# Optimization experiments

Measured on AMD Instinct MI355X. Metric: run time of the kernel, lower is better.

The kernel has to match this reference:

```python
import jax, jax.numpy as jnp
import numpy as np

N = 80          # grid points per side
L = 2.0         # domain size, grid spans [-L//2, L//2] = [-1, 1]
NG = 4          # num_gaussians; alpha has 4*NG entries (last NG unused, as in source)


def setup_inputs() -> dict:
    key = jax.random.key(0)
    k_alpha, = jax.random.split(key, 1)
    # amplitudes/centers in [0,1): keeps 1 + sum(a_i * gaussian) strictly positive
    alpha = jax.random.uniform(k_alpha, (4 * NG,), dtype=jnp.float32)

    # 5-point Laplacian stencil matrix, identical to the double loop in _assemble_lhs:
    # A = kron(I, T) + kron(T, I), T = tridiag(-1, 2, -1)
    T = 2.0 * np.eye(N) - np.eye(N, k=1) - np.eye(N, k=-1)
    A = np.kron(np.eye(N), T) + np.kron(T, np.eye(N))

    # rhs f = func(x, y) on the meshgrid, func = sin(pi x) sin(pi y)
    xs = np.linspace(-(L // 2), L // 2, N)
    X, Y = np.meshgrid(xs, xs, indexing='ij')
    f = np.sin(np.pi * X) * np.sin(np.pi * Y)

    return {
        'alpha': alpha,
        'A': jnp.asarray(A, dtype=jnp.float32),
        'f': jnp.asarray(f.reshape(-1), dtype=jnp.float32),
    }


def reference(alpha, A, f):
    # diffusion map: 1 + sum_i a_i * exp(-((x - cx_i)^2 + (y - cy_i)^2))
    xs = jnp.linspace(-(L // 2), L // 2, N, dtype=jnp.float32)
    X, Y = jnp.meshgrid(xs, xs, indexing='ij')          # (N, N)
    amps = alpha[:NG]
    cx = alpha[NG:2 * NG]
    cy = alpha[2 * NG:3 * NG]
    # (N, N, NG) gaussian basis, contracted against amplitudes
    g = jnp.exp(-((X[..., None] - cx) ** 2 + (Y[..., None] - cy) ** 2))
    dm = 1.0 + g @ amps                                  # (N, N)
    # torch broadcasting: dm (M,) * A (M, M) scales COLUMNS of A
    M = A * dm.reshape(-1)[None, :]
    return jnp.linalg.solve(M, f)
```

## Files before the change

### kernel.cpp

```cpp
#include <hip/hip_runtime.h>
#include <math.h>


#define NN   80
#define NP   81
#define RPW  4
#define NWG  (NN / RPW)
#define NTH  (RPW * NN)
#define PIF  3.14159265358979323846f

__device__ __forceinline__ void build_sin_table(float* tbl, int tid) {
    if (tid < 2 * NP) tbl[tid] = sinf(PIF * (float)tid / (float)NP);
}

__device__ __forceinline__ void build_S(float (*Sm)[NN], const float* tbl, int tid) {
    for (int p = tid; p < NN * NN; p += NTH) {
        const int k = p / NN, i = p - k * NN;
        Sm[k][i] = tbl[((k + 1) * (i + 1)) % (2 * NP)];
    }
}

__global__ __launch_bounds__(NTH) void poisson_phase1(
    const float* __restrict__ f, float* __restrict__ u2g)
{
    __shared__ __align__(16) float Sm[NN][NN];
    __shared__ __align__(16) float Fl[NN][NN];
    __shared__ float U1[RPW][NN];
    __shared__ float tbl[2 * NP];
    __shared__ float lam[NN];

    const int tid = threadIdx.x;
    const int wg  = blockIdx.x;

    build_sin_table(tbl, tid);
    if (tid < NN) {
        const float s = sinf(PIF * (float)(tid + 1) / (2.0f * (float)NP));
        lam[tid] = 4.0f * s * s;
    }
    for (int p = tid; p < NN * NN / 4; p += NTH)
        reinterpret_cast<float4*>(&Fl[0][0])[p] =
            reinterpret_cast<const float4*>(f)[p];
    __syncthreads();
    build_S(Sm, tbl, tid);
    __syncthreads();

    const int r = tid / NN;
    const int i = tid - r * NN;
    const int a = wg * RPW + r;

    float acc = 0.0f;
    #pragma unroll 8
    for (int k = 0; k < NN; ++k) acc += Sm[a][k] * Fl[k][i];
    U1[r][i] = acc;
    __syncthreads();

    float acc2 = 0.0f;
    #pragma unroll 8
    for (int k = 0; k < NN; ++k) acc2 += U1[r][k] * Sm[k][i];
    u2g[a * NN + i] = acc2 / (lam[a] + lam[i]);
}

__global__ __launch_bounds__(NTH) void poisson_phase2(
    const float* __restrict__ alpha, const float* __restrict__ u2g,
    float* __restrict__ out)
{
    __shared__ __align__(16) float Sm[NN][NN];
    __shared__ __align__(16) float U2[NN][NN];
    __shared__ float Tl[RPW][NN];
    __shared__ float tbl[2 * NP];
    __shared__ float gyl[4][NN];
    __shared__ float gxv[RPW][4];

    const int tid = threadIdx.x;
    const int wg  = blockIdx.x;

    build_sin_table(tbl, tid);
    for (int p = tid; p < NN * NN / 4; p += NTH)
        reinterpret_cast<float4*>(&U2[0][0])[p] =
            reinterpret_cast<const float4*>(u2g)[p];
    {
        const int k = tid / NN, j = tid - k * NN;
        const float yj = -1.0f + 2.0f * (float)j / 79.0f;
        const float d  = yj - alpha[8 + k];
        gyl[k][j] = __expf(-(d * d));
    }
    if (tid < RPW * 4) {
        const int r = tid / 4, k = tid - r * 4;
        const float xi = -1.0f + 2.0f * (float)(wg * RPW + r) / 79.0f;
        const float d  = xi - alpha[4 + k];
        gxv[r][k] = alpha[k] * __expf(-(d * d));
    }
    __syncthreads();
    build_S(Sm, tbl, tid);
    __syncthreads();

    const int r   = tid / NN;
    const int j   = tid - r * NN;
    const int row = wg * RPW + r;

    float t = 0.0f;
    #pragma unroll 8
    for (int a = 0; a < NN; ++a) t += Sm[row][a] * U2[a][j];
    Tl[r][j] = t;
    __syncthreads();

    float y = 0.0f;
    #pragma unroll 8
    for (int b = 0; b < NN; ++b) y += Tl[r][b] * Sm[b][j];

    float dm = 1.0f;
    #pragma unroll
    for (int k = 0; k < 4; ++k) dm += gxv[r][k] * gyl[k][j];

    const float scale = 4.0f / ((float)NP * (float)NP);
    out[row * NN + j] = y * scale / dm;
}

extern "C" void kernel_launch(void* const* d_in, const int* in_sizes, int n_in,
                              void* d_out, int out_size, void* d_ws, size_t ws_size,
                              hipStream_t stream) {
    const float* alpha = (const float*)d_in[0];
    const float* f = (const float*)d_in[2];
    float* out = (float*)d_out;
    float* u2  = (float*)d_ws;

    hipLaunchKernelGGL(poisson_phase1, dim3(NWG), dim3(NTH), 0, stream, f, u2);
    hipLaunchKernelGGL(poisson_phase2, dim3(NWG), dim3(NTH), 0, stream, alpha, u2, out);
}
```

Before: 16.06 us.

## Register-tile the DST matmuls with float4 2x4 micro-tiles and vectorize sine-matrix build

Each of the two small matrix products per workgroup now runs on 40 threads, each computing a 2x4 register tile with float4 LDS loads, instead of 320 threads each computing one scalar dot product. The sine-matrix build uses one thread per quarter-row, with an incremental modulo index replacing a per-element division and modulo. The global-to-LDS copy is issued before the table setup to overlap latency. This cuts LDS load traffic and index arithmetic, but leaves most threads idle during the matmuls, which reduces parallelism and latency hiding.

```diff
diff --git a/kernel.cpp b/kernel.cpp
--- a/kernel.cpp
+++ b/kernel.cpp
@@ -6,17 +6,50 @@
 #define NP   81
 #define RPW  4
 #define NWG  (NN / RPW)
-#define NTH  (RPW * NN)
+#define NTH  320
 #define PIF  3.14159265358979323846f
+
+__device__ __forceinline__ void gemm2x4(const float* __restrict__ row0,
+                                        const float* __restrict__ row1,
+                                        const float (*__restrict__ Cm)[NN],
+                                        int c4, float acc[2][4])
+{
+    #pragma unroll
+    for (int r = 0; r < 2; ++r)
+        #pragma unroll
+        for (int c = 0; c < 4; ++c) acc[r][c] = 0.0f;
+
+    #pragma unroll 4
+    for (int k4 = 0; k4 < NN; k4 += 4) {
+        const float4 a0 = *reinterpret_cast<const float4*>(row0 + k4);
+        const float4 a1 = *reinterpret_cast<const float4*>(row1 + k4);
+        const float4 b0 = *reinterpret_cast<const float4*>(&Cm[k4 + 0][c4]);
+        const float4 b1 = *reinterpret_cast<const float4*>(&Cm[k4 + 1][c4]);
+        const float4 b2 = *reinterpret_cast<const float4*>(&Cm[k4 + 2][c4]);
+        const float4 b3 = *reinterpret_cast<const float4*>(&Cm[k4 + 3][c4]);
+        acc[0][0] += a0.x*b0.x; acc[0][1] += a0.x*b0.y; acc[0][2] += a0.x*b0.z; acc[0][3] += a0.x*b0.w;
+        acc[0][0] += a0.y*b1.x; acc[0][1] += a0.y*b1.y; acc[0][2] += a0.y*b1.z; acc[0][3] += a0.y*b1.w;
+        acc[0][0] += a0.z*b2.x; acc[0][1] += a0.z*b2.y; acc[0][2] += a0.z*b2.z; acc[0][3] += a0.z*b2.w;
+        acc[0][0] += a0.w*b3.x; acc[0][1] += a0.w*b3.y; acc[0][2] += a0.w*b3.z; acc[0][3] += a0.w*b3.w;
+        acc[1][0] += a1.x*b0.x; acc[1][1] += a1.x*b0.y; acc[1][2] += a1.x*b0.z; acc[1][3] += a1.x*b0.w;
+        acc[1][0] += a1.y*b1.x; acc[1][1] += a1.y*b1.y; acc[1][2] += a1.y*b1.z; acc[1][3] += a1.y*b1.w;
+        acc[1][0] += a1.z*b2.x; acc[1][1] += a1.z*b2.y; acc[1][2] += a1.z*b2.z; acc[1][3] += a1.z*b2.w;
+        acc[1][0] += a1.w*b3.x; acc[1][1] += a1.w*b3.y; acc[1][2] += a1.w*b3.z; acc[1][3] += a1.w*b3.w;
+    }
+}
 
 __device__ __forceinline__ void build_sin_table(float* tbl, int tid) {
     if (tid < 2 * NP) tbl[tid] = sinf(PIF * (float)tid / (float)NP);
 }
 
 __device__ __forceinline__ void build_S(float (*Sm)[NN], const float* tbl, int tid) {
-    for (int p = tid; p < NN * NN; p += NTH) {
-        const int k = p / NN, i = p - k * NN;
-        Sm[k][i] = tbl[((k + 1) * (i + 1)) % (2 * NP)];
+    const int k = tid >> 2, q = tid & 3;
+    const int k1 = k + 1, base = q * 20;
+    int m = (k1 * (base + 1)) % (2 * NP);
+    #pragma unroll
+    for (int ii = 0; ii < 20; ++ii) {
+        Sm[k][base + ii] = tbl[m];
+        m += k1; if (m >= 2 * NP) m -= 2 * NP;
     }
 }
 
@@ -24,40 +57,53 @@
     const float* __restrict__ f, float* __restrict__ u2g)
 {
     __shared__ __align__(16) float Sm[NN][NN];
-    __shared__ __align__(16) float Fl[NN][NN];
-    __shared__ float U1[RPW][NN];
+    __shared__ __align__(16) float Wb[NN][NN];
+    __shared__ __align__(16) float Rw[RPW][NN];
     __shared__ float tbl[2 * NP];
     __shared__ float lam[NN];
 
     const int tid = threadIdx.x;
     const int wg  = blockIdx.x;
 
+    for (int p = tid; p < NN * NN / 4; p += NTH)
+        reinterpret_cast<float4*>(&Wb[0][0])[p] =
+            reinterpret_cast<const float4*>(f)[p];
     build_sin_table(tbl, tid);
     if (tid < NN) {
         const float s = sinf(PIF * (float)(tid + 1) / (2.0f * (float)NP));
         lam[tid] = 4.0f * s * s;
     }
-    for (int p = tid; p < NN * NN / 4; p += NTH)
-        reinterpret_cast<float4*>(&Fl[0][0])[p] =
-            reinterpret_cast<const float4*>(f)[p];
     __syncthreads();
     build_S(Sm, tbl, tid);
     __syncthreads();
 
-    const int r = tid / NN;
-    const int i = tid - r * NN;
-    const int a = wg * RPW + r;
+    const bool active = tid < 2 * 20;
+    const int r0 = (tid / 20) * 2;
+    const int c4 = (tid % 20) * 4;
+    const int a0 = wg * RPW + r0;
+    float acc[2][4];
 
-    float acc = 0.0f;
-    #pragma unroll 8
-    for (int k = 0; k < NN; ++k) acc += Sm[a][k] * Fl[k][i];
-    U1[r][i] = acc;
+    if (active) {
+        gemm2x4(&Sm[a0][0], &Sm[a0 + 1][0], Wb, c4, acc);
+        *reinterpret_cast<float4*>(&Rw[r0][c4]) =
+            make_float4(acc[0][0], acc[0][1], acc[0][2], acc[0][3]);
+        *reinterpret_cast<float4*>(&Rw[r0 + 1][c4]) =
+            make_float4(acc[1][0], acc[1][1], acc[1][2], acc[1][3]);
+    }
     __syncthreads();
 
-    float acc2 = 0.0f;
-    #pragma unroll 8
-    for (int k = 0; k < NN; ++k) acc2 += U1[r][k] * Sm[k][i];
-    u2g[a * NN + i] = acc2 / (lam[a] + lam[i]);
+    if (active) {
+        gemm2x4(&Rw[r0][0], &Rw[r0 + 1][0], Sm, c4, acc);
+        #pragma unroll
+        for (int r = 0; r < 2; ++r) {
+            const float la = lam[a0 + r];
+            *reinterpret_cast<float4*>(&u2g[(a0 + r) * NN + c4]) =
+                make_float4(acc[r][0] / (la + lam[c4 + 0]),
+                            acc[r][1] / (la + lam[c4 + 1]),
+                            acc[r][2] / (la + lam[c4 + 2]),
+                            acc[r][3] / (la + lam[c4 + 3]));
+        }
+    }
 }
 
 __global__ __launch_bounds__(NTH) void poisson_phase2(
@@ -65,8 +111,8 @@
     float* __restrict__ out)
 {
     __shared__ __align__(16) float Sm[NN][NN];
-    __shared__ __align__(16) float U2[NN][NN];
-    __shared__ float Tl[RPW][NN];
+    __shared__ __align__(16) float Wb[NN][NN];
+    __shared__ __align__(16) float Rw[RPW][NN];
     __shared__ float tbl[2 * NP];
     __shared__ float gyl[4][NN];
     __shared__ float gxv[RPW][4];
@@ -74,10 +120,10 @@
     const int tid = threadIdx.x;
     const int wg  = blockIdx.x;
 
+    for (int p = tid; p < NN * NN / 4; p += NTH)
+        reinterpret_cast<float4*>(&Wb[0][0])[p] =
+            reinterpret_cast<const float4*>(u2g)[p];
     build_sin_table(tbl, tid);
-    for (int p = tid; p < NN * NN / 4; p += NTH)
-        reinterpret_cast<float4*>(&U2[0][0])[p] =
-            reinterpret_cast<const float4*>(u2g)[p];
     {
         const int k = tid / NN, j = tid - k * NN;
         const float yj = -1.0f + 2.0f * (float)j / 79.0f;
@@ -85,7 +131,7 @@
         gyl[k][j] = __expf(-(d * d));
     }
     if (tid < RPW * 4) {
-        const int r = tid / 4, k = tid - r * 4;
+        const int r = tid / 4, k = tid & 3;
         const float xi = -1.0f + 2.0f * (float)(wg * RPW + r) / 79.0f;
         const float d  = xi - alpha[4 + k];
         gxv[r][k] = alpha[k] * __expf(-(d * d));
@@ -94,26 +140,38 @@
     build_S(Sm, tbl, tid);
     __syncthreads();
 
-    const int r   = tid / NN;
-    const int j   = tid - r * NN;
-    const int row = wg * RPW + r;
+    const bool active = tid < 2 * 20;
+    const int r0 = (tid / 20) * 2;
+    const int c4 = (tid % 20) * 4;
+    const int a0 = wg * RPW + r0;
+    float acc[2][4];
 
-    float t = 0.0f;
-    #pragma unroll 8
-    for (int a = 0; a < NN; ++a) t += Sm[row][a] * U2[a][j];
-    Tl[r][j] = t;
+    if (active) {
+        gemm2x4(&Sm[a0][0], &Sm[a0 + 1][0], Wb, c4, acc);
+        *reinterpret_cast<float4*>(&Rw[r0][c4]) =
+            make_float4(acc[0][0], acc[0][1], acc[0][2], acc[0][3]);
+        *reinterpret_cast<float4*>(&Rw[r0 + 1][c4]) =
+            make_float4(acc[1][0], acc[1][1], acc[1][2], acc[1][3]);
+    }
     __syncthreads();
 
-    float y = 0.0f;
-    #pragma unroll 8
-    for (int b = 0; b < NN; ++b) y += Tl[r][b] * Sm[b][j];
-
-    float dm = 1.0f;
-    #pragma unroll
-    for (int k = 0; k < 4; ++k) dm += gxv[r][k] * gyl[k][j];
-
-    const float scale = 4.0f / ((float)NP * (float)NP);
-    out[row * NN + j] = y * scale / dm;
+    if (active) {
+        gemm2x4(&Rw[r0][0], &Rw[r0 + 1][0], Sm, c4, acc);
+        const float scale = 4.0f / ((float)NP * (float)NP);
+        #pragma unroll
+        for (int r = 0; r < 2; ++r) {
+            float o[4];
+            #pragma unroll
+            for (int c = 0; c < 4; ++c) {
+                float dm = 1.0f;
+                #pragma unroll
+                for (int k = 0; k < 4; ++k) dm += gxv[r0 + r][k] * gyl[k][c4 + c];
+                o[c] = acc[r][c] * scale / dm;
+            }
+            *reinterpret_cast<float4*>(&out[(a0 + r) * NN + c4]) =
+                make_float4(o[0], o[1], o[2], o[3]);
+        }
+    }
 }
 
 extern "C" void kernel_launch(void* const* d_in, const int* in_sizes, int n_in,
```

New measurement: 16.51 us. 1.03x slower.
